# Kernel optimization log

Hardware: AMD Instinct MI355X
Metric: run time of the kernel (lower is better)

## Reference

```python
import jax, jax.numpy as jnp
import numpy as np


def setup_inputs() -> dict:
    key = jax.random.key(0)
    k1, k2 = jax.random.split(key)
    B, N, D = 4, 2048, 1024
    context = jax.random.normal(k1, (B, N, D), dtype=jnp.float32)
    # Dense(embedding_dim*3): kernel [D, 3D], bias [3D] (glorot-ish scale)
    W_qkv = jax.random.normal(k2, (D, 3 * D), dtype=jnp.float32) * (1.0 / np.sqrt(D))
    b_qkv = jnp.zeros((3 * D,), dtype=jnp.float32)
    return {"context": context, "W_qkv": W_qkv, "b_qkv": b_qkv}


def reference(context, W_qkv, b_qkv):
    B, N, D = context.shape
    qkv = context @ W_qkv + b_qkv                       # [B, N, 3D]
    q, k, v = jnp.split(qkv, 3, axis=-1)                # each [B, N, D]
    scores = jnp.einsum("bnd,bmd->bnm", q, k)           # [B, N, N]
    # Faithful quirk: original divides by sqrt(scores.shape[-1]) == sqrt(N)
    scores = scores / jnp.asarray(np.sqrt(N), dtype=scores.dtype)
    causal = jnp.tril(jnp.ones((N, N), dtype=jnp.float32))  # lower-triangular
    scores = jnp.where(causal == 0, -jnp.inf, scores)
    probs = jax.nn.softmax(scores, axis=-1)             # [B, N, N]
    out = jnp.einsum("bnm,bmd->bnd", probs, v)          # [B, N, D]
    return out
```

## Files before the change

kernel.cpp:

```cpp
#include <hip/hip_runtime.h>
#include <cstdint>
#include <cstddef>


typedef __attribute__((ext_vector_type(8))) __bf16 bf16x8;
typedef __attribute__((ext_vector_type(4))) float f32x4;

__device__ inline unsigned short f2bf(float f) {
  unsigned u = __float_as_uint(f);
  u = (u + 0x7FFFu + ((u >> 16) & 1u)) >> 16;
  return (unsigned short)u;
}

__device__ inline void gld16(const void* g, void* l) {
  __builtin_amdgcn_global_load_lds(
      (const __attribute__((address_space(1))) unsigned int*)g,
      (__attribute__((address_space(3))) unsigned int*)l, 16, 0, 0);
}

__device__ inline void compute_tiles(const unsigned short* As, const unsigned short* Bs,
                                     int lane, int ry, int rx, f32x4 acc[4][4]) {
#pragma unroll
  for (int kk = 0; kk < 64; kk += 32) {
    const int cbase = (kk >> 3) + (lane >> 4);
    const int csw = ((cbase ^ (lane & 7)) << 3);
    bf16x8 a[4], b[4];
#pragma unroll
    for (int mi = 0; mi < 4; mi++)
      a[mi] = *(const bf16x8*)&As[(ry + mi * 16 + (lane & 15)) * 64 + csw];
#pragma unroll
    for (int nj = 0; nj < 4; nj++)
      b[nj] = *(const bf16x8*)&Bs[(rx + nj * 16 + (lane & 15)) * 64 + csw];
#pragma unroll
    for (int mi = 0; mi < 4; mi++)
#pragma unroll
      for (int nj = 0; nj < 4; nj++)
        acc[mi][nj] = __builtin_amdgcn_mfma_f32_16x16x32_bf16(b[nj], a[mi], acc[mi][nj], 0, 0, 0);
  }
}

__device__ inline void mma_mainloop(unsigned short* As, unsigned short* Bs,
                                    const unsigned short* Abase, long strideA,
                                    const unsigned short* Bbase, long strideB,
                                    int kIters, f32x4 acc[4][4]) {
  const int lane = threadIdx.x & 63, wave = threadIdx.x >> 6;
  const int ry = (wave >> 1) * 64, rx = (wave & 1) * 64;
  const int lrow = lane >> 3;
  const int lcol = ((lane & 7) ^ lrow) * 8;
#pragma unroll
  for (int mi = 0; mi < 4; mi++)
#pragma unroll
    for (int nj = 0; nj < 4; nj++) acc[mi][nj] = (f32x4)(0.f);
  for (int kt = 0; kt < kIters; kt++) {
    const int k0 = kt * 64;
    __syncthreads();
#pragma unroll
    for (int c = 0; c < 4; c++) {
      const int q = wave * 4 + c;
      const int row = q * 8 + lrow;
      gld16(Abase + (size_t)row * strideA + k0 + lcol, &As[q * 512]);
      gld16(Bbase + (size_t)row * strideB + k0 + lcol, &Bs[q * 512]);
    }
    __syncthreads();
    compute_tiles(As, Bs, lane, ry, rx, acc);
  }
}

__device__ inline void compute_tiles64(const unsigned short* As, const unsigned short* Bs,
                                       int lane, int ry, int rx, f32x4 acc[4][2]) {
#pragma unroll
  for (int kk = 0; kk < 64; kk += 32) {
    const int cbase = (kk >> 3) + (lane >> 4);
    const int csw = ((cbase ^ (lane & 7)) << 3);
    bf16x8 a[4], b[2];
#pragma unroll
    for (int mi = 0; mi < 4; mi++)
      a[mi] = *(const bf16x8*)&As[(ry + mi * 16 + (lane & 15)) * 64 + csw];
#pragma unroll
    for (int nj = 0; nj < 2; nj++)
      b[nj] = *(const bf16x8*)&Bs[(rx + nj * 16 + (lane & 15)) * 64 + csw];
#pragma unroll
    for (int mi = 0; mi < 4; mi++)
#pragma unroll
      for (int nj = 0; nj < 2; nj++)
        acc[mi][nj] = __builtin_amdgcn_mfma_f32_16x16x32_bf16(b[nj], a[mi], acc[mi][nj], 0, 0, 0);
  }
}

__device__ inline void mma_mainloop64(unsigned short* As, unsigned short* Bs,
                                      const unsigned short* Abase, long strideA,
                                      const unsigned short* Bbase, long strideB,
                                      int kIters, f32x4 acc[4][2]) {
  const int lane = threadIdx.x & 63, wave = threadIdx.x >> 6;
  const int ry = (wave >> 1) * 64, rx = (wave & 1) * 32;
  const int lrow = lane >> 3;
  const int lcol = ((lane & 7) ^ lrow) * 8;
#pragma unroll
  for (int mi = 0; mi < 4; mi++)
#pragma unroll
    for (int nj = 0; nj < 2; nj++) acc[mi][nj] = (f32x4)(0.f);
  for (int kt = 0; kt < kIters; kt++) {
    const int k0 = kt * 64;
    __syncthreads();
#pragma unroll
    for (int c = 0; c < 4; c++) {
      const int q = wave * 4 + c;
      const int row = q * 8 + lrow;
      gld16(Abase + (size_t)row * strideA + k0 + lcol, &As[q * 512]);
    }
#pragma unroll
    for (int c = 0; c < 2; c++) {
      const int q = wave * 2 + c;
      const int row = q * 8 + lrow;
      gld16(Bbase + (size_t)row * strideB + k0 + lcol, &Bs[q * 512]);
    }
    __syncthreads();
    compute_tiles64(As, Bs, lane, ry, rx, acc);
  }
}

__global__ void k_prep(const float* __restrict__ x, unsigned short* __restrict__ y,
                       const float* __restrict__ W, unsigned short* __restrict__ Wt) {
  __shared__ unsigned short sm[64 * 65];
  const int bid = blockIdx.x;
  if (bid < 8192) {
    const int i = bid * 256 + threadIdx.x;
    float4 v = ((const float4*)x)[i];
    ushort4 o;
    o.x = f2bf(v.x); o.y = f2bf(v.y); o.z = f2bf(v.z); o.w = f2bf(v.w);
    ((ushort4*)y)[i] = o;
  } else {
    const int t = bid - 8192;
    const int n0 = (t % 48) * 64;
    const int k0 = (t / 48) * 64;
    for (int i = threadIdx.x; i < 4096; i += 256) {
      int r = i >> 6, c = i & 63;
      sm[c * 65 + r] = f2bf(W[(size_t)(k0 + r) * 3072 + n0 + c]);
    }
    __syncthreads();
    for (int i = threadIdx.x; i < 4096; i += 256) {
      int r = i >> 6, c = i & 63;
      Wt[(size_t)(n0 + r) * 1024 + k0 + c] = sm[r * 65 + c];
    }
  }
}


__global__ __launch_bounds__(256) void k_gemm_qk(const unsigned short* __restrict__ A,
                                                 const unsigned short* __restrict__ Wt,
                                                 const float* __restrict__ bias,
                                                 unsigned short* __restrict__ qk,
                                                 int mbase) {
  __shared__ unsigned short As[128 * 64];
  __shared__ unsigned short Bs[128 * 64];
  f32x4 acc[4][4];
  const int tN0 = blockIdx.x * 128;
  const int tM0 = mbase + blockIdx.y * 128;
  mma_mainloop(As, Bs, A + (size_t)tM0 * 1024, 1024, Wt + (size_t)tN0 * 1024, 1024, 16, acc);
  const int lane = threadIdx.x & 63, wave = threadIdx.x >> 6;
  const int ry = (wave >> 1) * 64, rx = (wave & 1) * 64;
  const int l16 = lane & 15, rq = lane >> 4;
#pragma unroll
  for (int mi = 0; mi < 4; mi++) {
    const int m = tM0 + ry + mi * 16 + l16;
#pragma unroll
    for (int nj = 0; nj < 4; nj++) {
      const int n = tN0 + rx + nj * 16 + rq * 4;
      const float4 bv = *(const float4*)&bias[n];
      ushort4 o;
      o.x = f2bf(acc[mi][nj][0] + bv.x);
      o.y = f2bf(acc[mi][nj][1] + bv.y);
      o.z = f2bf(acc[mi][nj][2] + bv.z);
      o.w = f2bf(acc[mi][nj][3] + bv.w);
      *(ushort4*)&qk[(size_t)m * 2048 + n] = o;
    }
  }
}

__global__ __launch_bounds__(256) void k_gemm_v(const unsigned short* __restrict__ A,
                                                const unsigned short* __restrict__ Wt,
                                                const float* __restrict__ bias,
                                                unsigned short* __restrict__ vT) {
  __shared__ unsigned short As[128 * 64];
  __shared__ unsigned short Bs[128 * 64];
  f32x4 acc[4][4];
  const int tN0 = blockIdx.x * 128;
  const int tM0 = blockIdx.y * 128;
  mma_mainloop(As, Bs, A + (size_t)tM0 * 1024, 1024,
               Wt + (size_t)(2048 + tN0) * 1024, 1024, 16, acc);
  int tM0v = tM0;
  asm volatile("" : "+v"(tM0v));
  const int lane = threadIdx.x & 63, wave = threadIdx.x >> 6;
  const int ry = (wave >> 1) * 64, rx = (wave & 1) * 64;
  const int l16 = lane & 15, rq = lane >> 4;
#pragma unroll
  for (int mi = 0; mi < 4; mi++) {
    const int m = tM0v + ry + mi * 16 + l16;
    const int b = m >> 11, ns = m & 2047;
#pragma unroll
    for (int nj = 0; nj < 4; nj++) {
      const int d0 = tN0 + rx + nj * 16 + rq * 4;
      const float4 bv = *(const float4*)&bias[2048 + d0];
#pragma unroll
      for (int r = 0; r < 4; r++)
        vT[((size_t)(b * 1024 + d0 + r)) * 2048 + ns] =
            f2bf(acc[mi][nj][r] + ((const float*)&bv)[r]);
    }
  }
}


__global__ __launch_bounds__(256) void k_scores(const unsigned short* __restrict__ qk,
                                                unsigned short* __restrict__ P,
                                                float* __restrict__ l, float scale) {
  __shared__ unsigned short As[128 * 64];
  __shared__ unsigned short Bs[64 * 64];
  const int t = blockIdx.x, b = blockIdx.z;
  int qb = (int)((sqrtf(4.0f * (float)t + 1.0f) - 1.0f) * 0.5f);
  while (qb * (qb + 1) > t) qb--;
  while ((qb + 1) * (qb + 2) <= t) qb++;
  const int kb2 = t - qb * (qb + 1);
  f32x4 acc[4][2];
  const unsigned short* Aq = qk + ((size_t)(b * 2048 + qb * 128)) * 2048;
  const unsigned short* Bk = qk + ((size_t)(b * 2048 + kb2 * 64)) * 2048 + 1024;
  mma_mainloop64(As, Bs, Aq, 2048, Bk, 2048, 16, acc);
  const int lane = threadIdx.x & 63, wave = threadIdx.x >> 6;
  const int ry = (wave >> 1) * 64, rx = (wave & 1) * 32;
  const int l16 = lane & 15, rq = lane >> 4;
  unsigned short* Pb = P + ((size_t)(b * 2048 + qb * 128)) * 2048 + (size_t)kb2 * 64;
  float* lb = l + b * 2048 + qb * 128;
#pragma unroll
  for (int mi = 0; mi < 4; mi++) {
    const int m_local = ry + mi * 16 + l16;
    const int qi = qb * 128 + m_local;
    float rowpart = 0.f;
#pragma unroll
    for (int nj = 0; nj < 2; nj++) {
      const int n_base = rx + nj * 16 + rq * 4;
      ushort4 o;
      float p;
#pragma unroll
      for (int r = 0; r < 4; r++) {
        const int kj = kb2 * 64 + n_base + r;
        p = (kj <= qi) ? __expf(acc[mi][nj][r] * scale) : 0.f;
        rowpart += p;
        ((unsigned short*)&o)[r] = f2bf(p);
      }
      *(ushort4*)&Pb[(size_t)m_local * 2048 + n_base] = o;
    }
    rowpart += __shfl_xor(rowpart, 16, 64);
    rowpart += __shfl_xor(rowpart, 32, 64);
    if (rq == 0) atomicAdd(&lb[m_local], rowpart);
  }
}

__global__ __launch_bounds__(256) void k_pv(const unsigned short* __restrict__ P,
                                            const unsigned short* __restrict__ vT,
                                            const float* __restrict__ l,
                                            float* __restrict__ out) {
  __shared__ unsigned short As[128 * 64];
  __shared__ unsigned short Bs[64 * 64];
  const int t = blockIdx.x;
  const int qb = 15 - (t >> 6);
  const int r = t & 63;
  const int db2 = r >> 2;
  const int b = r & 3;
  f32x4 acc[4][2];
  const unsigned short* Ap = P + ((size_t)(b * 2048 + qb * 128)) * 2048;
  const unsigned short* Bv = vT + ((size_t)(b * 1024 + db2 * 64)) * 2048;
  mma_mainloop64(As, Bs, Ap, 2048, Bv, 2048, (qb + 1) * 2, acc);
  const int lane = threadIdx.x & 63, wave = threadIdx.x >> 6;
  const int ry = (wave >> 1) * 64, rx = (wave & 1) * 32;
  const int l16 = lane & 15, rq = lane >> 4;
  const float* lb = l + b * 2048 + qb * 128;
  float* ob = out + ((size_t)(b * 2048 + qb * 128)) * 1024 + db2 * 64;
#pragma unroll
  for (int mi = 0; mi < 4; mi++) {
    const int m_local = ry + mi * 16 + l16;
    const float inv = 1.0f / lb[m_local];
#pragma unroll
    for (int nj = 0; nj < 2; nj++) {
      const int n_base = rx + nj * 16 + rq * 4;
      float4 o;
      o.x = acc[mi][nj][0] * inv;
      o.y = acc[mi][nj][1] * inv;
      o.z = acc[mi][nj][2] * inv;
      o.w = acc[mi][nj][3] * inv;
      *(float4*)&ob[(size_t)m_local * 1024 + n_base] = o;
    }
  }
}


extern "C" void kernel_launch(void* const* d_in, const int* in_sizes, int n_in,
                              void* d_out, int out_size, void* d_ws, size_t ws_size,
                              hipStream_t stream) {
  const float* ctx  = (const float*)d_in[0];
  const float* W    = (const float*)d_in[1];
  const float* bias = (const float*)d_in[2];
  float* out = (float*)d_out;

  char* ws = (char*)d_ws;
  unsigned short* Actx = (unsigned short*)(ws + 0);
  unsigned short* Wt   = (unsigned short*)(ws + 16777216);
  unsigned short* qk   = (unsigned short*)(ws + 23068672);
  unsigned short* vT   = (unsigned short*)(ws + 56623104);
  unsigned short* P    = (unsigned short*)(ws + 73400320);
  float*          lsum = (float*)(ws + 106954752);

  hipMemsetAsync(lsum, 0, 4 * 2048 * sizeof(float), stream);
  k_prep<<<8960, 256, 0, stream>>>(ctx, Actx, W, Wt);
  k_gemm_qk<<<dim3(16, 32), 256, 0, stream>>>(Actx, Wt, bias, qk, 0);
  k_gemm_qk<<<dim3(16, 32), 256, 0, stream>>>(Actx, Wt, bias, qk, 4096);
  k_gemm_v<<<dim3(8, 64), 256, 0, stream>>>(Actx, Wt, bias, vT);
  k_scores<<<dim3(272, 1, 4), 256, 0, stream>>>(qk, P, lsum, 0.022097086912079608f);
  k_pv<<<1024, 256, 0, stream>>>(P, vT, lsum, out);
}
```

Baseline: 242.8 us.

## Merge V projection with scores kernel and fold memset into prep

The lsum memset moves into an extra block of the prep kernel, and the prep conversion now handles four float4 per thread with fewer blocks. The two QK GEMM launches become one full-grid launch. The V projection GEMM and the causal scores kernel are fused into one heterogeneous launch, since neither depends on the other. This removes several launches and the tails between them, and lets the V GEMM blocks overlap with the scores blocks. The cost is a larger shared-memory footprint for the score blocks.

Result: no change. 238.7 us (-1.7%).

```diff
diff --git a/kernel.cpp b/kernel.cpp
--- a/kernel.cpp
+++ b/kernel.cpp
@@ -120,17 +120,21 @@
 }
 
 __global__ void k_prep(const float* __restrict__ x, unsigned short* __restrict__ y,
-                       const float* __restrict__ W, unsigned short* __restrict__ Wt) {
+                       const float* __restrict__ W, unsigned short* __restrict__ Wt,
+                       float* __restrict__ lsum) {
   __shared__ unsigned short sm[64 * 65];
   const int bid = blockIdx.x;
-  if (bid < 8192) {
-    const int i = bid * 256 + threadIdx.x;
-    float4 v = ((const float4*)x)[i];
-    ushort4 o;
-    o.x = f2bf(v.x); o.y = f2bf(v.y); o.z = f2bf(v.z); o.w = f2bf(v.w);
-    ((ushort4*)y)[i] = o;
-  } else {
-    const int t = bid - 8192;
+  if (bid < 2048) {
+#pragma unroll
+    for (int k = 0; k < 4; k++) {
+      const int i = bid * 1024 + k * 256 + threadIdx.x;
+      float4 v = ((const float4*)x)[i];
+      ushort4 o;
+      o.x = f2bf(v.x); o.y = f2bf(v.y); o.z = f2bf(v.z); o.w = f2bf(v.w);
+      ((ushort4*)y)[i] = o;
+    }
+  } else if (bid < 2816) {
+    const int t = bid - 2048;
     const int n0 = (t % 48) * 64;
     const int k0 = (t / 48) * 64;
     for (int i = threadIdx.x; i < 4096; i += 256) {
@@ -142,20 +146,22 @@
       int r = i >> 6, c = i & 63;
       Wt[(size_t)(n0 + r) * 1024 + k0 + c] = sm[r * 65 + c];
     }
-  }
-}
-
+  } else {
+#pragma unroll
+    for (int k = 0; k < 8; k++)
+      ((float4*)lsum)[k * 256 + threadIdx.x] = (float4)(0.f);
+  }
+}
 
 __global__ __launch_bounds__(256) void k_gemm_qk(const unsigned short* __restrict__ A,
                                                  const unsigned short* __restrict__ Wt,
                                                  const float* __restrict__ bias,
-                                                 unsigned short* __restrict__ qk,
-                                                 int mbase) {
+                                                 unsigned short* __restrict__ qk) {
   __shared__ unsigned short As[128 * 64];
   __shared__ unsigned short Bs[128 * 64];
   f32x4 acc[4][4];
   const int tN0 = blockIdx.x * 128;
-  const int tM0 = mbase + blockIdx.y * 128;
+  const int tM0 = blockIdx.y * 128;
   mma_mainloop(As, Bs, A + (size_t)tM0 * 1024, 1024, Wt + (size_t)tN0 * 1024, 1024, 16, acc);
   const int lane = threadIdx.x & 63, wave = threadIdx.x >> 6;
   const int ry = (wave >> 1) * 64, rx = (wave & 1) * 64;
@@ -177,80 +183,79 @@
   }
 }
 
-__global__ __launch_bounds__(256) void k_gemm_v(const unsigned short* __restrict__ A,
-                                                const unsigned short* __restrict__ Wt,
-                                                const float* __restrict__ bias,
-                                                unsigned short* __restrict__ vT) {
-  __shared__ unsigned short As[128 * 64];
-  __shared__ unsigned short Bs[128 * 64];
-  f32x4 acc[4][4];
-  const int tN0 = blockIdx.x * 128;
-  const int tM0 = blockIdx.y * 128;
-  mma_mainloop(As, Bs, A + (size_t)tM0 * 1024, 1024,
-               Wt + (size_t)(2048 + tN0) * 1024, 1024, 16, acc);
-  int tM0v = tM0;
-  asm volatile("" : "+v"(tM0v));
-  const int lane = threadIdx.x & 63, wave = threadIdx.x >> 6;
-  const int ry = (wave >> 1) * 64, rx = (wave & 1) * 64;
-  const int l16 = lane & 15, rq = lane >> 4;
-#pragma unroll
-  for (int mi = 0; mi < 4; mi++) {
-    const int m = tM0v + ry + mi * 16 + l16;
-    const int b = m >> 11, ns = m & 2047;
-#pragma unroll
-    for (int nj = 0; nj < 4; nj++) {
-      const int d0 = tN0 + rx + nj * 16 + rq * 4;
-      const float4 bv = *(const float4*)&bias[2048 + d0];
-#pragma unroll
-      for (int r = 0; r < 4; r++)
-        vT[((size_t)(b * 1024 + d0 + r)) * 2048 + ns] =
-            f2bf(acc[mi][nj][r] + ((const float*)&bv)[r]);
-    }
-  }
-}
-
-
-__global__ __launch_bounds__(256) void k_scores(const unsigned short* __restrict__ qk,
-                                                unsigned short* __restrict__ P,
-                                                float* __restrict__ l, float scale) {
-  __shared__ unsigned short As[128 * 64];
-  __shared__ unsigned short Bs[64 * 64];
-  const int t = blockIdx.x, b = blockIdx.z;
-  int qb = (int)((sqrtf(4.0f * (float)t + 1.0f) - 1.0f) * 0.5f);
-  while (qb * (qb + 1) > t) qb--;
-  while ((qb + 1) * (qb + 2) <= t) qb++;
-  const int kb2 = t - qb * (qb + 1);
-  f32x4 acc[4][2];
-  const unsigned short* Aq = qk + ((size_t)(b * 2048 + qb * 128)) * 2048;
-  const unsigned short* Bk = qk + ((size_t)(b * 2048 + kb2 * 64)) * 2048 + 1024;
-  mma_mainloop64(As, Bs, Aq, 2048, Bk, 2048, 16, acc);
-  const int lane = threadIdx.x & 63, wave = threadIdx.x >> 6;
-  const int ry = (wave >> 1) * 64, rx = (wave & 1) * 32;
-  const int l16 = lane & 15, rq = lane >> 4;
-  unsigned short* Pb = P + ((size_t)(b * 2048 + qb * 128)) * 2048 + (size_t)kb2 * 64;
-  float* lb = l + b * 2048 + qb * 128;
-#pragma unroll
-  for (int mi = 0; mi < 4; mi++) {
-    const int m_local = ry + mi * 16 + l16;
-    const int qi = qb * 128 + m_local;
-    float rowpart = 0.f;
-#pragma unroll
-    for (int nj = 0; nj < 2; nj++) {
-      const int n_base = rx + nj * 16 + rq * 4;
-      ushort4 o;
-      float p;
-#pragma unroll
-      for (int r = 0; r < 4; r++) {
-        const int kj = kb2 * 64 + n_base + r;
-        p = (kj <= qi) ? __expf(acc[mi][nj][r] * scale) : 0.f;
-        rowpart += p;
-        ((unsigned short*)&o)[r] = f2bf(p);
+__global__ __launch_bounds__(256) void k_vscores(
+    const unsigned short* __restrict__ A, const unsigned short* __restrict__ Wt,
+    const float* __restrict__ bias, unsigned short* __restrict__ vT,
+    const unsigned short* __restrict__ qk, unsigned short* __restrict__ P,
+    float* __restrict__ l, float scale) {
+  __shared__ unsigned short smem[16384];
+  unsigned short* As = smem;
+  unsigned short* Bs = smem + 8192;
+  const int bid = blockIdx.x;
+  const int lane = threadIdx.x & 63, wave = threadIdx.x >> 6;
+  if (bid < 512) {
+    f32x4 acc[4][4];
+    const int tN0 = (bid & 7) * 128;
+    const int tM0 = (bid >> 3) * 128;
+    mma_mainloop(As, Bs, A + (size_t)tM0 * 1024, 1024,
+                 Wt + (size_t)(2048 + tN0) * 1024, 1024, 16, acc);
+    int tM0v = tM0;
+    asm volatile("" : "+v"(tM0v));
+    const int ry = (wave >> 1) * 64, rx = (wave & 1) * 64;
+    const int l16 = lane & 15, rq = lane >> 4;
+#pragma unroll
+    for (int mi = 0; mi < 4; mi++) {
+      const int m = tM0v + ry + mi * 16 + l16;
+      const int b = m >> 11, ns = m & 2047;
+#pragma unroll
+      for (int nj = 0; nj < 4; nj++) {
+        const int d0 = tN0 + rx + nj * 16 + rq * 4;
+        const float4 bv = *(const float4*)&bias[2048 + d0];
+#pragma unroll
+        for (int r = 0; r < 4; r++)
+          vT[((size_t)(b * 1024 + d0 + r)) * 2048 + ns] =
+              f2bf(acc[mi][nj][r] + ((const float*)&bv)[r]);
       }
-      *(ushort4*)&Pb[(size_t)m_local * 2048 + n_base] = o;
-    }
-    rowpart += __shfl_xor(rowpart, 16, 64);
-    rowpart += __shfl_xor(rowpart, 32, 64);
-    if (rq == 0) atomicAdd(&lb[m_local], rowpart);
+    }
+  } else {
+    const int idx = bid - 512;
+    const int b = idx & 3;
+    const int t = idx >> 2;
+    int qb = (int)((sqrtf(4.0f * (float)t + 1.0f) - 1.0f) * 0.5f);
+    while (qb * (qb + 1) > t) qb--;
+    while ((qb + 1) * (qb + 2) <= t) qb++;
+    const int kb2 = t - qb * (qb + 1);
+    f32x4 acc[4][2];
+    const unsigned short* Aq = qk + ((size_t)(b * 2048 + qb * 128)) * 2048;
+    const unsigned short* Bk = qk + ((size_t)(b * 2048 + kb2 * 64)) * 2048 + 1024;
+    mma_mainloop64(As, Bs, Aq, 2048, Bk, 2048, 16, acc);
+    const int ry = (wave >> 1) * 64, rx = (wave & 1) * 32;
+    const int l16 = lane & 15, rq = lane >> 4;
+    unsigned short* Pb = P + ((size_t)(b * 2048 + qb * 128)) * 2048 + (size_t)kb2 * 64;
+    float* lb = l + b * 2048 + qb * 128;
+#pragma unroll
+    for (int mi = 0; mi < 4; mi++) {
+      const int m_local = ry + mi * 16 + l16;
+      const int qi = qb * 128 + m_local;
+      float rowpart = 0.f;
+#pragma unroll
+      for (int nj = 0; nj < 2; nj++) {
+        const int n_base = rx + nj * 16 + rq * 4;
+        ushort4 o;
+        float p;
+#pragma unroll
+        for (int r = 0; r < 4; r++) {
+          const int kj = kb2 * 64 + n_base + r;
+          p = (kj <= qi) ? __expf(acc[mi][nj][r] * scale) : 0.f;
+          rowpart += p;
+          ((unsigned short*)&o)[r] = f2bf(p);
+        }
+        *(ushort4*)&Pb[(size_t)m_local * 2048 + n_base] = o;
+      }
+      rowpart += __shfl_xor(rowpart, 16, 64);
+      rowpart += __shfl_xor(rowpart, 32, 64);
+      if (rq == 0) atomicAdd(&lb[m_local], rowpart);
+    }
   }
 }
 
@@ -308,11 +313,9 @@
   unsigned short* P    = (unsigned short*)(ws + 73400320);
   float*          lsum = (float*)(ws + 106954752);
 
-  hipMemsetAsync(lsum, 0, 4 * 2048 * sizeof(float), stream);
-  k_prep<<<8960, 256, 0, stream>>>(ctx, Actx, W, Wt);
-  k_gemm_qk<<<dim3(16, 32), 256, 0, stream>>>(Actx, Wt, bias, qk, 0);
-  k_gemm_qk<<<dim3(16, 32), 256, 0, stream>>>(Actx, Wt, bias, qk, 4096);
-  k_gemm_v<<<dim3(8, 64), 256, 0, stream>>>(Actx, Wt, bias, vT);
-  k_scores<<<dim3(272, 1, 4), 256, 0, stream>>>(qk, P, lsum, 0.022097086912079608f);
+  k_prep<<<2817, 256, 0, stream>>>(ctx, Actx, W, Wt, lsum);
+  k_gemm_qk<<<dim3(16, 64), 256, 0, stream>>>(Actx, Wt, bias, qk);
+  k_vscores<<<1600, 256, 0, stream>>>(Actx, Wt, bias, vT, qk, P, lsum,
+                                      0.022097086912079608f);
   k_pv<<<1024, 256, 0, stream>>>(P, vT, lsum, out);
 }
```
